# Optimization experiments

Measured on AMD Instinct MI355X. Metric: run time of the kernel, lower is better.

## Reference

```python
import jax, jax.numpy as jnp
import numpy as np

EPS = 1e-8            # torch cosine_similarity eps
RECENCY_WEIGHT = 0.3  # retrieve() default
NOVELTY_SCALE = 10.0  # _compute_novelty divides min dist by 10

B, N, D, K = 32, 1_000_000, 128, 16


def setup_inputs() -> dict:
    key = jax.random.key(0)
    ks = jax.random.split(key, 6)
    query = jax.random.normal(ks[0], (B, D), dtype=jnp.float32)
    memory = jax.random.normal(ks[1], (N, D), dtype=jnp.float32)
    importance = jax.random.uniform(ks[2], (N,), dtype=jnp.float32)
    timestamps = jnp.sort(jax.random.randint(ks[3], (N,), 0, N).astype(jnp.int32))
    Wq = jax.random.normal(ks[4], (D, D), dtype=jnp.float32) / jnp.sqrt(jnp.float32(D))
    bq = jax.random.normal(ks[5], (D,), dtype=jnp.float32) * 0.01
    return {
        "query": query,
        "memory": memory,
        "importance": importance,
        "timestamps": timestamps,
        "Wq": Wq,
        "bq": bq,
        "current_time": N,
        "k": K,
    }


def reference(query, memory, importance, timestamps, Wq, bq, current_time, k):
    # query_net: Linear(item_dim, item_dim)
    q = query @ Wq.T + bq                              # [B, D]

    # --- batched cosine similarity against the whole bank (replaces Python loop) ---
    q_norm = jnp.sqrt(jnp.sum(q * q, axis=-1, keepdims=True))          # [B, 1]
    m_norm = jnp.sqrt(jnp.sum(memory * memory, axis=-1, keepdims=True))  # [N, 1]
    dots = jnp.einsum("bd,nd->bn", q, memory)                          # [B, N]
    sim = dots / jnp.maximum(q_norm * m_norm.T, EPS)                   # [B, N]

    # recency = (timestamp + 1) / (current_time + 1)
    recency = (timestamps.astype(jnp.float32) + 1.0) / (jnp.float32(current_time) + 1.0)  # [N]

    score = (1.0 - RECENCY_WEIGHT) * sim + RECENCY_WEIGHT * recency[None, :]
    score = score * (0.5 + 0.5 * importance)[None, :]                  # [B, N]

    topk_scores, topk_idx = jax.lax.top_k(score, k)                    # [B, k]

    # --- novelty: min L2 distance from q to any stored vector, capped at 1 ---
    # ||q - m||^2 = ||q||^2 + ||m||^2 - 2 q.m
    d2 = q_norm**2 + m_norm.T**2 - 2.0 * dots                          # [B, N]
    min_dist = jnp.sqrt(jnp.maximum(jnp.min(d2, axis=-1), 0.0))        # [B]
    novelty = jnp.minimum(1.0, min_dist / NOVELTY_SCALE)               # [B]

    return topk_scores, topk_idx, novelty
```

## Files before the change

### kernel.cpp

```cpp
#include <hip/hip_runtime.h>
#include <float.h>

#define BQ 32
#define DIM 128
#define TOPK 16
#define G1 768
#define T1 256
#define T2 256
#define NCAND (G1*16)

__global__ void ph0_qproj(const float* __restrict__ query, const float* __restrict__ Wq,
                          const float* __restrict__ bq,
                          float* __restrict__ qT, float* __restrict__ qn2,
                          float* __restrict__ sinvq)
{
    const int b = blockIdx.x;
    const int d = threadIdx.x;
    float s = bq[d];
    #pragma unroll 8
    for (int kk = 0; kk < DIM; ++kk)
        s = fmaf(query[b * DIM + kk], Wq[d * DIM + kk], s);
    qT[d * BQ + b] = s;
    __shared__ float red[DIM];
    red[d] = s * s;
    __syncthreads();
    for (int off = DIM / 2; off >= 1; off >>= 1) {
        if (d < off) red[d] += red[d + off];
        __syncthreads();
    }
    if (d == 0) {
        qn2[b] = red[0];
        sinvq[b] = 1.0f / sqrtf(red[0]);
    }
}

__global__ __launch_bounds__(T1, 3) void ph1_scan(
    const float* __restrict__ mem, const float* __restrict__ imp,
    const int* __restrict__ tsp, const float* __restrict__ qT,
    const float* __restrict__ sinvq, const float* __restrict__ qn2,
    const int* __restrict__ ctp,
    float* __restrict__ cand_sc, int* __restrict__ cand_ix,
    float* __restrict__ minD_ws, int N, int C, int iters)
{
    __shared__ float trbuf[4][64 * 36];

    const int tid = threadIdx.x;
    const int wave = tid >> 6;
    const int lane = tid & 63;
    const int g = blockIdx.x;
    const int n0 = g * C;
    const int n1 = (n0 + C < N) ? (n0 + C) : N;
    const int qsel = lane & 31;
    const int hsel = lane >> 5;

    const float invct = 1.0f / ((float)(*ctp) + 1.0f);
    const float sq = sinvq[qsel];
    const float qn2s = qn2[qsel];

    float top_s[TOPK];
    int   top_i[TOPK];
    #pragma unroll
    for (int j = 0; j < TOPK; ++j) { top_s[j] = -FLT_MAX; top_i[j] = 0; }
    float mind = FLT_MAX;

    float* tb = &trbuf[wave][0];

    for (int it = 0; it < iters; ++it) {
        const int rowbase = n0 + it * (4 * 64) + wave * 64;
        if (rowbase < n1) {
            const int row = rowbase + lane;
            const bool valid = row < n1;
            const int rc = valid ? row : (n1 - 1);
            const float4* mrow = (const float4*)(mem + (size_t)rc * DIM);

            float acc[BQ];
            #pragma unroll
            for (int b = 0; b < BQ; ++b) acc[b] = 0.0f;
            float m2 = 0.0f;

            float4 pf[4];
            #pragma unroll
            for (int j = 0; j < 4; ++j) pf[j] = mrow[j];

            #pragma unroll 1
            for (int dd = 0; dd < 8; ++dd) {
                #pragma unroll
                for (int jj = 0; jj < 4; ++jj) {
                    const int d4 = dd * 4 + jj;
                    float4 u = pf[jj];
                    const int nx = (d4 + 4 < 32) ? (d4 + 4) : 31;
                    pf[jj] = mrow[nx];
                    m2 = fmaf(u.x, u.x, fmaf(u.y, u.y, fmaf(u.z, u.z, fmaf(u.w, u.w, m2))));
                    const float* qp = qT + d4 * (4 * BQ);
                    #pragma unroll
                    for (int b = 0; b < BQ; ++b) acc[b] = fmaf(u.x, qp[b], acc[b]);
                    #pragma unroll
                    for (int b = 0; b < BQ; ++b) acc[b] = fmaf(u.y, qp[BQ + b], acc[b]);
                    #pragma unroll
                    for (int b = 0; b < BQ; ++b) acc[b] = fmaf(u.z, qp[2 * BQ + b], acc[b]);
                    #pragma unroll
                    for (int b = 0; b < BQ; ++b) acc[b] = fmaf(u.w, qp[3 * BQ + b], acc[b]);
                }
            }

            const float invm = rsqrtf(m2);
            const float recn = ((float)tsp[rc] + 1.0f) * invct;
            const float impf = fmaf(0.5f, imp[rc], 0.5f);
            const float k1 = 0.7f * invm * impf;
            const float k2 = 0.3f * recn * impf;

            #pragma unroll
            for (int b = 0; b < BQ; ++b) tb[lane * 36 + b] = acc[b];
            tb[lane * 36 + 32] = k1;
            tb[lane * 36 + 33] = k2;
            tb[lane * 36 + 34] = m2;
            tb[lane * 36 + 35] = valid ? 1.0f : -1.0f;

            #pragma unroll 1
            for (int j = 0; j < 32; ++j) {
                const int rr = (hsel << 5) + j;
                const float a = tb[rr * 36 + qsel];
                const float4 kk = *(const float4*)&tb[rr * 36 + 32];
                const float score = fmaf(a, kk.x * sq, kk.y);
                const float d2 = fmaf(-2.0f, a, qn2s + kk.z);
                if (kk.w > 0.0f) {
                    mind = fminf(mind, d2);
                    if (score > top_s[TOPK - 1]) {
                        float cs = score; int ci = rowbase + rr;
                        #pragma unroll
                        for (int p = 0; p < TOPK; ++p) {
                            const bool gt = cs > top_s[p];
                            const float tv = top_s[p]; const int tx = top_i[p];
                            top_s[p] = gt ? cs : tv;  top_i[p] = gt ? ci : tx;
                            cs = gt ? tv : cs;        ci = gt ? tx : ci;
                        }
                    }
                }
            }
        }
    }

    __syncthreads();
    float* dsc = &trbuf[0][0];
    int*   dix = (int*)(dsc + T1 * TOPK);
    float* dmn = dsc + 2 * T1 * TOPK;
    #pragma unroll
    for (int j = 0; j < TOPK; ++j) {
        dsc[tid * TOPK + j] = top_s[j];
        dix[tid * TOPK + j] = top_i[j];
    }
    dmn[tid] = mind;
    __syncthreads();

    for (int qq = 0; qq < 8; ++qq) {
        const int q = wave * 8 + qq;
        float sc2[2]; int ix2[2];
        #pragma unroll
        for (int s = 0; s < 2; ++s) {
            const int c = lane * 2 + s;
            const int L = (c >> 4) * 32 + q;
            const int slot = c & 15;
            sc2[s] = dsc[L * TOPK + slot];
            ix2[s] = dix[L * TOPK + slot];
        }
        float lm = (sc2[0] >= sc2[1]) ? sc2[0] : sc2[1];
        int   ls = (sc2[0] >= sc2[1]) ? 0 : 1;
        for (int r = 0; r < TOPK; ++r) {
            float v = lm; int we = lane;
            #pragma unroll
            for (int off = 32; off >= 1; off >>= 1) {
                const float ov = __shfl_xor(v, off);
                const int   oe = __shfl_xor(we, off);
                if (ov > v || (ov == v && oe < we)) { v = ov; we = oe; }
            }
            if (lane == we) {
                cand_sc[(g * 32 + q) * TOPK + r] = lm;
                cand_ix[(g * 32 + q) * TOPK + r] = ix2[ls];
                sc2[ls] = -FLT_MAX;
                lm = (sc2[0] >= sc2[1]) ? sc2[0] : sc2[1];
                ls = (sc2[0] >= sc2[1]) ? 0 : 1;
            }
        }
    }

    if (tid < 32) {
        float m = FLT_MAX;
        #pragma unroll
        for (int l = 0; l < 8; ++l) m = fminf(m, dmn[l * 32 + tid]);
        minD_ws[g * 32 + tid] = m;
    }
}

__global__ void ph2_final(const float* __restrict__ cand_sc, const int* __restrict__ cand_ix,
                          const float* __restrict__ minD_ws, float* __restrict__ out, int G)
{
    __shared__ float ssc[NCAND];
    __shared__ float shv[4];
    __shared__ int   she[4];
    __shared__ float smin[T2];

    const int q = blockIdx.x;
    const int tid = threadIdx.x;
    const int wave = tid >> 6;
    const int lane = tid & 63;

    for (int e = tid; e < NCAND; e += T2)
        ssc[e] = cand_sc[(e >> 4) * (32 * TOPK) + q * TOPK + (e & 15)];
    __syncthreads();

    float lm = ssc[tid]; int le = tid;
    for (int s = 1; s < NCAND / T2; ++s) {
        const int e = s * T2 + tid;
        const float v = ssc[e];
        if (v > lm) { lm = v; le = e; }
    }

    for (int r = 0; r < TOPK; ++r) {
        float v = lm; int e = le;
        #pragma unroll
        for (int off = 32; off >= 1; off >>= 1) {
            const float ov = __shfl_xor(v, off);
            const int   oe = __shfl_xor(e, off);
            if (ov > v || (ov == v && oe < e)) { v = ov; e = oe; }
        }
        if (lane == 0) { shv[wave] = v; she[wave] = e; }
        __syncthreads();
        float bv = shv[0]; int be = she[0];
        #pragma unroll
        for (int w2 = 1; w2 < 4; ++w2) {
            const float wv = shv[w2]; const int wе2 = she[w2];
            if (wv > bv || (wv == bv && wе2 < be)) { bv = wv; be = wе2; }
        }
        if (le == be) {
            out[q * TOPK + r] = bv;
            const int gix = cand_ix[(be >> 4) * (32 * TOPK) + q * TOPK + (be & 15)];
            out[BQ * TOPK + q * TOPK + r] = (float)gix;
            ssc[le] = -FLT_MAX;
            lm = ssc[tid]; le = tid;
            for (int s = 1; s < NCAND / T2; ++s) {
                const int e2 = s * T2 + tid;
                const float v2 = ssc[e2];
                if (v2 > lm) { lm = v2; le = e2; }
            }
        }
        __syncthreads();
    }

    float m = FLT_MAX;
    for (int g2 = tid; g2 < G; g2 += T2) m = fminf(m, minD_ws[g2 * 32 + q]);
    smin[tid] = m;
    __syncthreads();
    for (int off = T2 / 2; off >= 1; off >>= 1) {
        if (tid < off) smin[tid] = fminf(smin[tid], smin[tid + off]);
        __syncthreads();
    }
    if (tid == 0) {
        const float md = sqrtf(fmaxf(smin[0], 0.0f));
        out[2 * BQ * TOPK + q] = fminf(1.0f, md * 0.1f);
    }
}

extern "C" void kernel_launch(void* const* d_in, const int* in_sizes, int n_in,
                              void* d_out, int out_size, void* d_ws, size_t ws_size,
                              hipStream_t stream) {
    const float* query      = (const float*)d_in[0];
    const float* memory     = (const float*)d_in[1];
    const float* importance = (const float*)d_in[2];
    const int*   timestamps = (const int*)d_in[3];
    const float* Wq         = (const float*)d_in[4];
    const float* bq         = (const float*)d_in[5];
    const int*   ctp        = (const int*)d_in[6];
    const int N = in_sizes[2];

    float* ws      = (float*)d_ws;
    float* qT      = ws;
    float* qn2     = ws + 4096;
    float* sinvq   = ws + 4128;
    float* cand_sc = ws + 4352;
    int*   cand_ix = (int*)(ws + 4352 + G1 * 32 * TOPK);
    float* minD_ws = ws + 4352 + 2 * G1 * 32 * TOPK;

    const int C = (N + G1 - 1) / G1;
    const int iters = (C + (4 * 64) - 1) / (4 * 64);

    ph0_qproj<<<BQ, DIM, 0, stream>>>(query, Wq, bq, qT, qn2, sinvq);
    ph1_scan<<<G1, T1, 0, stream>>>(memory, importance, timestamps, qT, sinvq, qn2,
                                    ctp, cand_sc, cand_ix, minD_ws, N, C, iters);
    ph2_final<<<BQ, T2, 0, stream>>>(cand_sc, cand_ix, minD_ws, (float*)d_out, G1);
}
```

Baseline: 931.7 us.

## Compute scan dot products with bf16x3 split MFMA instead of scalar FMA

Replaces the per-thread scalar FP32 FMA dot-product loop in the scan kernel with 32x32x16 bf16 MFMA instructions. Both the query and memory operands are split into three bf16 parts, and six cross-products are accumulated to approximate FP32 accuracy. The scoring epilogue now reads per-row constants from a small shared buffer instead of transposing the full accumulator through LDS. The grid is reduced to 512 blocks with an occupancy hint of 2. The split costs extra conversion ALU work per element, and accuracy relies on the three-term split being close enough to FP32 for top-k ordering.

```diff
diff --git a/kernel.cpp b/kernel.cpp
--- a/kernel.cpp
+++ b/kernel.cpp
@@ -4,10 +4,36 @@
 #define BQ 32
 #define DIM 128
 #define TOPK 16
-#define G1 768
+#define G1 512
 #define T1 256
 #define T2 256
 #define NCAND (G1*16)
+
+typedef float f32x16 __attribute__((ext_vector_type(16)));
+typedef __bf16 bf16x8 __attribute__((ext_vector_type(8)));
+typedef unsigned int u32x4 __attribute__((ext_vector_type(4)));
+
+static __device__ __forceinline__ unsigned cvt_pk_bf16(float a, float b) {
+    unsigned r;
+    asm("v_cvt_pk_bf16_f32 %0, %1, %2" : "=v"(r) : "v"(a), "v"(b));
+    return r;
+}
+
+static __device__ __forceinline__ void split3(float f0, float f1,
+                                              unsigned &h01, unsigned &m01, unsigned &l01) {
+    h01 = cvt_pk_bf16(f0, f1);
+    float r0 = f0 - __uint_as_float(h01 << 16);
+    float r1 = f1 - __uint_as_float(h01 & 0xffff0000u);
+    m01 = cvt_pk_bf16(r0, r1);
+    float s0 = r0 - __uint_as_float(m01 << 16);
+    float s1 = r1 - __uint_as_float(m01 & 0xffff0000u);
+    l01 = cvt_pk_bf16(s0, s1);
+}
+
+static __device__ __forceinline__ f32x16 mfma32(u32x4 a, u32x4 b, f32x16 c) {
+    return __builtin_amdgcn_mfma_f32_32x32x16_bf16(
+        __builtin_bit_cast(bf16x8, a), __builtin_bit_cast(bf16x8, b), c, 0, 0, 0);
+}
 
 __global__ void ph0_qproj(const float* __restrict__ query, const float* __restrict__ Wq,
                           const float* __restrict__ bq,
@@ -34,116 +60,117 @@
     }
 }
 
-__global__ __launch_bounds__(T1, 3) void ph1_scan(
+__global__ __launch_bounds__(T1, 2) void ph1_scan(
     const float* __restrict__ mem, const float* __restrict__ imp,
     const int* __restrict__ tsp, const float* __restrict__ qT,
     const float* __restrict__ sinvq, const float* __restrict__ qn2,
     const int* __restrict__ ctp,
     float* __restrict__ cand_sc, int* __restrict__ cand_ix,
-    float* __restrict__ minD_ws, int N, int C, int iters)
+    float* __restrict__ minD_ws, int N, int C)
 {
-    __shared__ float trbuf[4][64 * 36];
-
-    const int tid = threadIdx.x;
+    __shared__ float dsc[T1 * TOPK];
+    __shared__ int   dix[T1 * TOPK];
+    __shared__ float dmn[T1];
+    __shared__ float4 cbuf[4][BQ];
+
+    const int tid  = threadIdx.x;
     const int wave = tid >> 6;
     const int lane = tid & 63;
+    const int qsel = lane & 31;
+    const int hsel = lane >> 5;
     const int g = blockIdx.x;
     const int n0 = g * C;
     const int n1 = (n0 + C < N) ? (n0 + C) : N;
-    const int qsel = lane & 31;
-    const int hsel = lane >> 5;
 
     const float invct = 1.0f / ((float)(*ctp) + 1.0f);
-    const float sq = sinvq[qsel];
+    const float sq   = sinvq[qsel];
     const float qn2s = qn2[qsel];
 
-    float top_s[TOPK];
-    int   top_i[TOPK];
+    u32x4 Bh[8], Bm[8], Bl[8];
+    #pragma unroll
+    for (int t = 0; t < 8; ++t) {
+        float x[8];
+        #pragma unroll
+        for (int j = 0; j < 8; ++j)
+            x[j] = qT[(t * 16 + hsel * 8 + j) * BQ + qsel];
+        #pragma unroll
+        for (int p = 0; p < 4; ++p) {
+            unsigned h, m, l;
+            split3(x[2 * p], x[2 * p + 1], h, m, l);
+            Bh[t][p] = h; Bm[t][p] = m; Bl[t][p] = l;
+        }
+    }
+
+    float top_s[TOPK]; int top_i[TOPK];
     #pragma unroll
     for (int j = 0; j < TOPK; ++j) { top_s[j] = -FLT_MAX; top_i[j] = 0; }
     float mind = FLT_MAX;
 
-    float* tb = &trbuf[wave][0];
-
-    for (int it = 0; it < iters; ++it) {
-        const int rowbase = n0 + it * (4 * 64) + wave * 64;
-        if (rowbase < n1) {
-            const int row = rowbase + lane;
-            const bool valid = row < n1;
-            const int rc = valid ? row : (n1 - 1);
-            const float4* mrow = (const float4*)(mem + (size_t)rc * DIM);
-
-            float acc[BQ];
+    const int rlast = n1 - 1;
+    for (int rb = n0 + wave * 32; rb < n1; rb += 4 * 32) {
+        const int arow = rb + qsel;
+        const int arc  = (arow < rlast) ? arow : rlast;
+        const float* rp = mem + (size_t)arc * DIM + hsel * 8;
+
+        f32x16 acc = { 0.f, 0.f, 0.f, 0.f, 0.f, 0.f, 0.f, 0.f,
+                       0.f, 0.f, 0.f, 0.f, 0.f, 0.f, 0.f, 0.f };
+        float m2p = 0.0f;
+
+        #pragma unroll
+        for (int t = 0; t < 8; ++t) {
+            const float4 xa = *(const float4*)(rp + t * 16);
+            const float4 xb = *(const float4*)(rp + t * 16 + 4);
+            const float xs[8] = { xa.x, xa.y, xa.z, xa.w, xb.x, xb.y, xb.z, xb.w };
+            u32x4 Ah, Am, Al;
             #pragma unroll
-            for (int b = 0; b < BQ; ++b) acc[b] = 0.0f;
-            float m2 = 0.0f;
-
-            float4 pf[4];
-            #pragma unroll
-            for (int j = 0; j < 4; ++j) pf[j] = mrow[j];
-
-            #pragma unroll 1
-            for (int dd = 0; dd < 8; ++dd) {
-                #pragma unroll
-                for (int jj = 0; jj < 4; ++jj) {
-                    const int d4 = dd * 4 + jj;
-                    float4 u = pf[jj];
-                    const int nx = (d4 + 4 < 32) ? (d4 + 4) : 31;
-                    pf[jj] = mrow[nx];
-                    m2 = fmaf(u.x, u.x, fmaf(u.y, u.y, fmaf(u.z, u.z, fmaf(u.w, u.w, m2))));
-                    const float* qp = qT + d4 * (4 * BQ);
+            for (int p = 0; p < 4; ++p) {
+                unsigned h, m, l;
+                split3(xs[2 * p], xs[2 * p + 1], h, m, l);
+                Ah[p] = h; Am[p] = m; Al[p] = l;
+                m2p = fmaf(xs[2 * p], xs[2 * p], m2p);
+                m2p = fmaf(xs[2 * p + 1], xs[2 * p + 1], m2p);
+            }
+            acc = mfma32(Al, Bh[t], acc);
+            acc = mfma32(Am, Bm[t], acc);
+            acc = mfma32(Ah, Bl[t], acc);
+            acc = mfma32(Am, Bh[t], acc);
+            acc = mfma32(Ah, Bm[t], acc);
+            acc = mfma32(Ah, Bh[t], acc);
+        }
+
+        const float m2full = m2p + __shfl_xor(m2p, 32);
+        const int crow = rb + qsel;
+        const int crc  = (crow < rlast) ? crow : rlast;
+        const float impf = fmaf(0.5f, imp[crc], 0.5f);
+        const float recn = ((float)tsp[crc] + 1.0f) * invct;
+        const float invm = rsqrtf(m2full);
+        cbuf[wave][qsel] = make_float4(0.7f * invm * impf,
+                                       0.3f * recn * impf,
+                                       m2full,
+                                       (crow < n1) ? 1.0f : -1.0f);
+        #pragma unroll
+        for (int reg = 0; reg < 16; ++reg) {
+            const int r = (reg & 3) + 8 * (reg >> 2) + 4 * hsel;
+            const float4 cc = cbuf[wave][r];
+            const float dot = acc[reg];
+            const float score = fmaf(dot, cc.x * sq, cc.y);
+            const float d2 = fmaf(-2.0f, dot, qn2s + cc.z);
+            if (cc.w > 0.0f) {
+                mind = fminf(mind, d2);
+                if (score > top_s[TOPK - 1]) {
+                    float cs = score; int ci = rb + r;
                     #pragma unroll
-                    for (int b = 0; b < BQ; ++b) acc[b] = fmaf(u.x, qp[b], acc[b]);
-                    #pragma unroll
-                    for (int b = 0; b < BQ; ++b) acc[b] = fmaf(u.y, qp[BQ + b], acc[b]);
-                    #pragma unroll
-                    for (int b = 0; b < BQ; ++b) acc[b] = fmaf(u.z, qp[2 * BQ + b], acc[b]);
-                    #pragma unroll
-                    for (int b = 0; b < BQ; ++b) acc[b] = fmaf(u.w, qp[3 * BQ + b], acc[b]);
-                }
-            }
-
-            const float invm = rsqrtf(m2);
-            const float recn = ((float)tsp[rc] + 1.0f) * invct;
-            const float impf = fmaf(0.5f, imp[rc], 0.5f);
-            const float k1 = 0.7f * invm * impf;
-            const float k2 = 0.3f * recn * impf;
-
-            #pragma unroll
-            for (int b = 0; b < BQ; ++b) tb[lane * 36 + b] = acc[b];
-            tb[lane * 36 + 32] = k1;
-            tb[lane * 36 + 33] = k2;
-            tb[lane * 36 + 34] = m2;
-            tb[lane * 36 + 35] = valid ? 1.0f : -1.0f;
-
-            #pragma unroll 1
-            for (int j = 0; j < 32; ++j) {
-                const int rr = (hsel << 5) + j;
-                const float a = tb[rr * 36 + qsel];
-                const float4 kk = *(const float4*)&tb[rr * 36 + 32];
-                const float score = fmaf(a, kk.x * sq, kk.y);
-                const float d2 = fmaf(-2.0f, a, qn2s + kk.z);
-                if (kk.w > 0.0f) {
-                    mind = fminf(mind, d2);
-                    if (score > top_s[TOPK - 1]) {
-                        float cs = score; int ci = rowbase + rr;
-                        #pragma unroll
-                        for (int p = 0; p < TOPK; ++p) {
-                            const bool gt = cs > top_s[p];
-                            const float tv = top_s[p]; const int tx = top_i[p];
-                            top_s[p] = gt ? cs : tv;  top_i[p] = gt ? ci : tx;
-                            cs = gt ? tv : cs;        ci = gt ? tx : ci;
-                        }
+                    for (int p = 0; p < TOPK; ++p) {
+                        const bool gt = cs > top_s[p];
+                        const float tv = top_s[p]; const int tx = top_i[p];
+                        top_s[p] = gt ? cs : tv;  top_i[p] = gt ? ci : tx;
+                        cs = gt ? tv : cs;        ci = gt ? tx : ci;
                     }
                 }
             }
         }
     }
 
-    __syncthreads();
-    float* dsc = &trbuf[0][0];
-    int*   dix = (int*)(dsc + T1 * TOPK);
-    float* dmn = dsc + 2 * T1 * TOPK;
     #pragma unroll
     for (int j = 0; j < TOPK; ++j) {
         dsc[tid * TOPK + j] = top_s[j];
@@ -228,8 +255,8 @@
         float bv = shv[0]; int be = she[0];
         #pragma unroll
         for (int w2 = 1; w2 < 4; ++w2) {
-            const float wv = shv[w2]; const int wе2 = she[w2];
-            if (wv > bv || (wv == bv && wе2 < be)) { bv = wv; be = wе2; }
+            const float wv = shv[w2]; const int we2 = she[w2];
+            if (wv > bv || (wv == bv && we2 < be)) { bv = wv; be = we2; }
         }
         if (le == be) {
             out[q * TOPK + r] = bv;
@@ -281,10 +308,9 @@
     float* minD_ws = ws + 4352 + 2 * G1 * 32 * TOPK;
 
     const int C = (N + G1 - 1) / G1;
-    const int iters = (C + (4 * 64) - 1) / (4 * 64);
 
     ph0_qproj<<<BQ, DIM, 0, stream>>>(query, Wq, bq, qT, qn2, sinvq);
     ph1_scan<<<G1, T1, 0, stream>>>(memory, importance, timestamps, qT, sinvq, qn2,
-                                    ctp, cand_sc, cand_ix, minD_ws, N, C, iters);
+                                    ctp, cand_sc, cand_ix, minD_ws, N, C);
     ph2_final<<<BQ, T2, 0, stream>>>(cand_sc, cand_ix, minD_ws, (float*)d_out, G1);
 }
```

New measurement: 889.8 us. 4.5% less time.
